# Performance work log

Measured on AMD Instinct MI355X. Metric: run time of the kernel, lower is better.

## Reference

```python
import jax, jax.numpy as jnp
import numpy as np

B, N, C = 1, 2048, 64


def setup_inputs() -> dict:
    key = jax.random.key(0)
    ks = jax.random.split(key, 7)
    X = jax.random.normal(ks[0], (B, N, 3), jnp.float32)
    embs = jax.random.normal(ks[1], (B, N, C), jnp.float32)
    w0 = jax.random.uniform(ks[2], (N,), jnp.float32)
    s0 = jax.random.uniform(ks[3], (N,), jnp.float32)
    paired_mask = jax.random.uniform(ks[4], (B, N, N), jnp.float32)
    # params: xavier_uniform(gain=0.1) + 1.0  ->  ~1.0 with small spread
    depth_factor = 1.0 + 0.05 * jax.random.normal(ks[5], (2 * C, 1), jnp.float32)
    radius_factor = 1.0 + 0.05 * jax.random.normal(ks[6], (2 * C, 1), jnp.float32)
    return {"X": X, "embs": embs, "w0": w0, "s0": s0, "paired_mask": paired_mask,
            "depth_factor": depth_factor, "radius_factor": radius_factor}


def reference(X, embs, w0, s0, paired_mask, depth_factor, radius_factor):
    c = embs.shape[-1]
    # pairwise distances; torch adds 1e-6 per coordinate before the sum
    V = X[:, None, :, :] - X[:, :, None, :]            # (B,N,N,3), V[b,i,j] = X[b,j]-X[b,i]
    D = jnp.sqrt(jnp.sum(V * V + 1e-6, axis=-1))       # (B,N,N)

    # emb_ij[b,i,j] = concat(embs[b,j], embs[b,i]); matmul with (2C,1) factor
    # splits exactly into two per-node dot products broadcast over the pair grid,
    # so the (B,N,N,2C) concat tensor never needs to be materialized.
    sig_r = jax.nn.sigmoid(embs @ radius_factor[c:, 0][:, None] .squeeze(-1)[:, :, None]
                           + (embs @ radius_factor[:c, 0][:, None]).squeeze(-1)[:, None, :]) if False else \
        jax.nn.sigmoid(jnp.einsum('bnc,c->bn', embs, radius_factor[c:, 0])[:, :, None]
                       + jnp.einsum('bnc,c->bn', embs, radius_factor[:c, 0])[:, None, :])  # (B,N,N)
    sig_d = jax.nn.sigmoid(jnp.einsum('bnc,c->bn', embs, depth_factor[c:, 0])[:, :, None]
                           + jnp.einsum('bnc,c->bn', embs, depth_factor[:c, 0])[:, None, :])  # (B,N,N)

    s0_ij = (s0[None, :] + s0[:, None])[None, None]    # (1,1,N,N)
    s = s0_ij * (0.8 * sig_r + 0.4)                    # (B,B(=1),N,N)

    repl = 5.0 * jnp.exp(-0.3 * D * D * D) * paired_mask   # (B,N,N)

    Dm = D - s                                          # (1,1,N,N) via broadcast
    attr = (jnp.exp(-(Dm - 0.3) * (Dm - 0.3))
            + jnp.exp(-3.0 * Dm * Dm)
            + jnp.exp(-10.0 * Dm * Dm)) / 3.0 * paired_mask

    w0_ij = jnp.sqrt(w0[None, :] * w0[:, None] + 1e-6)[None, None]  # (1,1,N,N)
    w = w0_ij * (sig_d + 0.5)

    Etotal = jnp.sum(-w * attr + repl[None])            # scalar
    Etotal = jnp.where(jnp.isnan(Etotal), jnp.float32(1e-6), Etotal)
    return Etotal
```

## Files before the change

### kernel.cpp

```cpp
#include <hip/hip_runtime.h>

#define NN 2048
#define CC 64

__global__ void prep_kernel(const float* __restrict__ embs,
                            const float* __restrict__ depth_factor,
                            const float* __restrict__ radius_factor,
                            const float* __restrict__ s0,
                            const float* __restrict__ w0,
                            float4* __restrict__ pj,
                            float* __restrict__ ih,
                            float* __restrict__ out) {
    int gid = blockIdx.x * blockDim.x + threadIdx.x;
    if (gid == 0) out[0] = 0.0f;

    int node = gid >> 6;
    int lane = threadIdx.x & 63;
    if (node >= NN) return;

    float e  = embs[node * CC + lane];
    float rl = e * radius_factor[lane];
    float rh = e * radius_factor[CC + lane];
    float dl = e * depth_factor[lane];
    float dh = e * depth_factor[CC + lane];

    #pragma unroll
    for (int off = 32; off > 0; off >>= 1) {
        rl += __shfl_down(rl, off, 64);
        rh += __shfl_down(rh, off, 64);
        dl += __shfl_down(dl, off, 64);
        dh += __shfl_down(dh, off, 64);
    }
    if (lane == 0) {
        pj[node] = make_float4(__expf(-rl), __expf(-dl),
                               s0[node], __builtin_amdgcn_sqrtf(w0[node]));
        ih[node]      = __expf(-rh);
        ih[NN + node] = __expf(-dh);
    }
}

__device__ __forceinline__ float pair_e(float xj, float yj, float zj,
                                        float4 p, float m,
                                        float xi, float yi, float zi,
                                        float Eri, float Edi,
                                        float s0i, float swi) {
    float dx = xj - xi, dy = yj - yi, dz = zj - zi;
    float d2 = fmaf(dx, dx, fmaf(dy, dy, fmaf(dz, dz, 3e-6f)));
    float D  = __builtin_amdgcn_sqrtf(d2);

    float sig_r = __builtin_amdgcn_rcpf(fmaf(Eri, p.x, 1.0f));
    float sig_d = __builtin_amdgcn_rcpf(fmaf(Edi, p.y, 1.0f));

    float s  = (s0i + p.z) * fmaf(0.8f, sig_r, 0.4f);
    float Dm = D - s;

    float repl = 5.0f * __expf(-0.3f * d2 * D);

    float e1 = __expf(-Dm * Dm);
    float g  = __expf(fmaf(0.6f, Dm, -0.09f));
    float e2 = e1 * e1;
    float e4 = e2 * e2;
    float e8 = e4 * e4;
    float attr3 = fmaf(e1, g, e2 * e1) + e8 * e2;

    float w = swi * p.w * (sig_d + 0.5f);

    return m * fmaf(-w * (1.0f / 3.0f), attr3, repl);
}

__global__ __launch_bounds__(256) void pair_energy_kernel(
        const float* __restrict__ X,
        const float* __restrict__ mask,
        const float4* __restrict__ pj,
        const float* __restrict__ ih,
        float* __restrict__ out) {
    const int i0 = 2 * blockIdx.x;
    const int i1 = i0 + 1;

    const float x0 = X[3 * i0], y0 = X[3 * i0 + 1], z0 = X[3 * i0 + 2];
    const float x1 = X[3 * i1], y1 = X[3 * i1 + 1], z1 = X[3 * i1 + 2];
    const float Er0 = ih[i0],      Er1 = ih[i1];
    const float Ed0 = ih[NN + i0], Ed1 = ih[NN + i1];
    const float4 q0 = pj[i0], q1 = pj[i1];

    const float4* __restrict__ mrow0 = (const float4*)(mask + (size_t)i0 * NN);
    const float4* __restrict__ mrow1 = (const float4*)(mask + (size_t)i1 * NN);
    const float4* __restrict__ X4    = (const float4*)X;

    float acc = 0.0f;
    #pragma unroll
    for (int it = 0; it < NN / (4 * 256); ++it) {
        int j4 = threadIdx.x + it * 256;
        float4 m0 = mrow0[j4];
        float4 m1 = mrow1[j4];
        float4 xa = X4[3 * j4];
        float4 xb = X4[3 * j4 + 1];
        float4 xc = X4[3 * j4 + 2];
        float4 p0 = pj[4 * j4];
        float4 p1 = pj[4 * j4 + 1];
        float4 p2 = pj[4 * j4 + 2];
        float4 p3 = pj[4 * j4 + 3];

        acc += pair_e(xa.x, xa.y, xa.z, p0, m0.x, x0, y0, z0, Er0, Ed0, q0.z, q0.w);
        acc += pair_e(xa.w, xb.x, xb.y, p1, m0.y, x0, y0, z0, Er0, Ed0, q0.z, q0.w);
        acc += pair_e(xb.z, xb.w, xc.x, p2, m0.z, x0, y0, z0, Er0, Ed0, q0.z, q0.w);
        acc += pair_e(xc.y, xc.z, xc.w, p3, m0.w, x0, y0, z0, Er0, Ed0, q0.z, q0.w);

        acc += pair_e(xa.x, xa.y, xa.z, p0, m1.x, x1, y1, z1, Er1, Ed1, q1.z, q1.w);
        acc += pair_e(xa.w, xb.x, xb.y, p1, m1.y, x1, y1, z1, Er1, Ed1, q1.z, q1.w);
        acc += pair_e(xb.z, xb.w, xc.x, p2, m1.z, x1, y1, z1, Er1, Ed1, q1.z, q1.w);
        acc += pair_e(xc.y, xc.z, xc.w, p3, m1.w, x1, y1, z1, Er1, Ed1, q1.z, q1.w);
    }

    #pragma unroll
    for (int off = 32; off > 0; off >>= 1) acc += __shfl_down(acc, off, 64);

    __shared__ float red[4];
    int lane = threadIdx.x & 63;
    int wid  = threadIdx.x >> 6;
    if (lane == 0) red[wid] = acc;
    __syncthreads();
    if (threadIdx.x == 0) {
        atomicAdd(out, red[0] + red[1] + red[2] + red[3]);
    }
}

extern "C" void kernel_launch(void* const* d_in, const int* in_sizes, int n_in,
                              void* d_out, int out_size, void* d_ws, size_t ws_size,
                              hipStream_t stream) {
    const float* X             = (const float*)d_in[0];
    const float* embs          = (const float*)d_in[1];
    const float* w0            = (const float*)d_in[2];
    const float* s0            = (const float*)d_in[3];
    const float* paired_mask   = (const float*)d_in[4];
    const float* depth_factor  = (const float*)d_in[5];
    const float* radius_factor = (const float*)d_in[6];

    float*  out = (float*)d_out;
    float4* pj  = (float4*)d_ws;
    float*  ih  = (float*)d_ws + 4 * NN;

    prep_kernel<<<dim3(NN / 4), dim3(256), 0, stream>>>(
        embs, depth_factor, radius_factor, s0, w0, pj, ih, out);

    pair_energy_kernel<<<dim3(NN / 2), dim3(256), 0, stream>>>(
        X, paired_mask, pj, ih, out);
}
```

Measured before the change: 93.03 us.

## Tile pair kernel as 4 rows by 1024 columns and share one reciprocal

The pair kernel now gives each block four i-rows and half of the j-range (a 2D grid). Each thread loads its j-side data (X, pj) once and reuses it across four rows, with all four mask loads issued up front for more memory-level parallelism. The two sigmoid reciprocals are merged into a single rcp of their product plus two multiplies. The trade is a slight rounding risk from the product and a different register and occupancy profile.

```diff
diff --git a/kernel.cpp b/kernel.cpp
--- a/kernel.cpp
+++ b/kernel.cpp
@@ -48,8 +48,11 @@
     float d2 = fmaf(dx, dx, fmaf(dy, dy, fmaf(dz, dz, 3e-6f)));
     float D  = __builtin_amdgcn_sqrtf(d2);
 
-    float sig_r = __builtin_amdgcn_rcpf(fmaf(Eri, p.x, 1.0f));
-    float sig_d = __builtin_amdgcn_rcpf(fmaf(Edi, p.y, 1.0f));
+    float a = fmaf(Eri, p.x, 1.0f);
+    float b = fmaf(Edi, p.y, 1.0f);
+    float rinv = __builtin_amdgcn_rcpf(a * b);
+    float sig_r = rinv * b;
+    float sig_d = rinv * a;
 
     float s  = (s0i + p.z) * fmaf(0.8f, sig_r, 0.4f);
     float Dm = D - s;
@@ -74,42 +77,35 @@
         const float4* __restrict__ pj,
         const float* __restrict__ ih,
         float* __restrict__ out) {
-    const int i0 = 2 * blockIdx.x;
-    const int i1 = i0 + 1;
+    const int i0 = 4 * blockIdx.x;
+    const int j4 = (blockIdx.y << 8) + threadIdx.x;
 
-    const float x0 = X[3 * i0], y0 = X[3 * i0 + 1], z0 = X[3 * i0 + 2];
-    const float x1 = X[3 * i1], y1 = X[3 * i1 + 1], z1 = X[3 * i1 + 2];
-    const float Er0 = ih[i0],      Er1 = ih[i1];
-    const float Ed0 = ih[NN + i0], Ed1 = ih[NN + i1];
-    const float4 q0 = pj[i0], q1 = pj[i1];
-
-    const float4* __restrict__ mrow0 = (const float4*)(mask + (size_t)i0 * NN);
-    const float4* __restrict__ mrow1 = (const float4*)(mask + (size_t)i1 * NN);
-    const float4* __restrict__ X4    = (const float4*)X;
+    const float4* __restrict__ X4 = (const float4*)X;
+    float4 m0 = ((const float4*)(mask + (size_t)(i0 + 0) * NN))[j4];
+    float4 m1 = ((const float4*)(mask + (size_t)(i0 + 1) * NN))[j4];
+    float4 m2 = ((const float4*)(mask + (size_t)(i0 + 2) * NN))[j4];
+    float4 m3 = ((const float4*)(mask + (size_t)(i0 + 3) * NN))[j4];
+    float4 xa = X4[3 * j4];
+    float4 xb = X4[3 * j4 + 1];
+    float4 xc = X4[3 * j4 + 2];
+    float4 p0 = pj[4 * j4];
+    float4 p1 = pj[4 * j4 + 1];
+    float4 p2 = pj[4 * j4 + 2];
+    float4 p3 = pj[4 * j4 + 3];
 
     float acc = 0.0f;
     #pragma unroll
-    for (int it = 0; it < NN / (4 * 256); ++it) {
-        int j4 = threadIdx.x + it * 256;
-        float4 m0 = mrow0[j4];
-        float4 m1 = mrow1[j4];
-        float4 xa = X4[3 * j4];
-        float4 xb = X4[3 * j4 + 1];
-        float4 xc = X4[3 * j4 + 2];
-        float4 p0 = pj[4 * j4];
-        float4 p1 = pj[4 * j4 + 1];
-        float4 p2 = pj[4 * j4 + 2];
-        float4 p3 = pj[4 * j4 + 3];
+    for (int r = 0; r < 4; ++r) {
+        const int i = i0 + r;
+        const float xi = X[3 * i], yi = X[3 * i + 1], zi = X[3 * i + 2];
+        const float Eri = ih[i], Edi = ih[NN + i];
+        const float4 qi = pj[i];
+        const float4 mr = (r == 0) ? m0 : (r == 1) ? m1 : (r == 2) ? m2 : m3;
 
-        acc += pair_e(xa.x, xa.y, xa.z, p0, m0.x, x0, y0, z0, Er0, Ed0, q0.z, q0.w);
-        acc += pair_e(xa.w, xb.x, xb.y, p1, m0.y, x0, y0, z0, Er0, Ed0, q0.z, q0.w);
-        acc += pair_e(xb.z, xb.w, xc.x, p2, m0.z, x0, y0, z0, Er0, Ed0, q0.z, q0.w);
-        acc += pair_e(xc.y, xc.z, xc.w, p3, m0.w, x0, y0, z0, Er0, Ed0, q0.z, q0.w);
-
-        acc += pair_e(xa.x, xa.y, xa.z, p0, m1.x, x1, y1, z1, Er1, Ed1, q1.z, q1.w);
-        acc += pair_e(xa.w, xb.x, xb.y, p1, m1.y, x1, y1, z1, Er1, Ed1, q1.z, q1.w);
-        acc += pair_e(xb.z, xb.w, xc.x, p2, m1.z, x1, y1, z1, Er1, Ed1, q1.z, q1.w);
-        acc += pair_e(xc.y, xc.z, xc.w, p3, m1.w, x1, y1, z1, Er1, Ed1, q1.z, q1.w);
+        acc += pair_e(xa.x, xa.y, xa.z, p0, mr.x, xi, yi, zi, Eri, Edi, qi.z, qi.w);
+        acc += pair_e(xa.w, xb.x, xb.y, p1, mr.y, xi, yi, zi, Eri, Edi, qi.z, qi.w);
+        acc += pair_e(xb.z, xb.w, xc.x, p2, mr.z, xi, yi, zi, Eri, Edi, qi.z, qi.w);
+        acc += pair_e(xc.y, xc.z, xc.w, p3, mr.w, xi, yi, zi, Eri, Edi, qi.z, qi.w);
     }
 
     #pragma unroll
@@ -143,6 +139,6 @@
     prep_kernel<<<dim3(NN / 4), dim3(256), 0, stream>>>(
         embs, depth_factor, radius_factor, s0, w0, pj, ih, out);
 
-    pair_energy_kernel<<<dim3(NN / 2), dim3(256), 0, stream>>>(
+    pair_energy_kernel<<<dim3(NN / 4, 2), dim3(256), 0, stream>>>(
         X, paired_mask, pj, ih, out);
 }
```

After: 92.07 us, median of 2. No clear change (-1.0%).
